# Optimization experiments

Measured on AMD Instinct MI355X. Metric: run time of the kernel, lower is better.

## Reference

```python
import jax, jax.numpy as jnp
import numpy as np

B_SZ = 16
L = 256
D_MODEL = 256
D_STATE = 16
D_CONV = 4
EXPAND = 2
D_INNER = EXPAND * D_MODEL  # 512
DT_RANK = (D_MODEL + 15) // 16  # 16
TARGET_LEN = 16


def setup_inputs() -> dict:
    key = jax.random.key(0)
    ks = jax.random.split(key, 10)
    s = 0.02
    x = jax.random.normal(ks[0], (B_SZ, D_MODEL, L), dtype=jnp.float32)
    W_in = jax.random.normal(ks[1], (2 * D_INNER, D_MODEL), dtype=jnp.float32) * s
    conv_w = jax.random.normal(ks[2], (D_INNER, D_CONV), dtype=jnp.float32) * s
    conv_b = jax.random.normal(ks[3], (D_INNER,), dtype=jnp.float32) * s
    W_x = jax.random.normal(ks[4], (DT_RANK + 2 * D_STATE, D_INNER), dtype=jnp.float32) * s
    W_dt = jax.random.normal(ks[5], (D_INNER, DT_RANK), dtype=jnp.float32) * s
    b_dt = jax.random.normal(ks[6], (D_INNER,), dtype=jnp.float32) * s
    # canonical Mamba A init: A_log = log(1..d_state) per channel
    A_log = jnp.log(jnp.tile(jnp.arange(1, D_STATE + 1, dtype=jnp.float32), (D_INNER, 1)))
    Dp = jnp.ones((D_INNER,), dtype=jnp.float32)
    W_out = jax.random.normal(ks[7], (D_MODEL, D_INNER), dtype=jnp.float32) * s
    return {"x": x, "W_in": W_in, "conv_w": conv_w, "conv_b": conv_b,
            "W_x": W_x, "W_dt": W_dt, "b_dt": b_dt, "A_log": A_log,
            "Dp": Dp, "W_out": W_out}


def _selective_scan(u, delta, A, Bm, Cm, Dp):
    # u, delta: [B,L,d_in]; Bm, Cm: [B,L,N]; A: [d_in,N]; Dp: [d_in]
    dA = jnp.exp(delta[..., None] * A)                                  # [B,L,d_in,N]
    dBu = delta[..., None] * Bm[:, :, None, :] * u[..., None]           # [B,L,d_in,N]

    def step(h, t):
        dA_t, dBu_t, C_t = t                                            # [B,d_in,N],[B,d_in,N],[B,N]
        h = dA_t * h + dBu_t
        y = jnp.einsum('bdn,bn->bd', h, C_t)
        return h, y

    h0 = jnp.zeros((u.shape[0], u.shape[2], A.shape[1]), u.dtype)
    _, ys = jax.lax.scan(step, h0,
                         (dA.transpose(1, 0, 2, 3), dBu.transpose(1, 0, 2, 3),
                          Cm.transpose(1, 0, 2)))
    return ys.transpose(1, 0, 2) + u * Dp                               # [B,L,d_in]


def _mamba(xt, W_in, conv_w, conv_b, W_x, W_dt, b_dt, A_log, Dp, W_out):
    # xt: [B,L,D_MODEL]
    xz = xt @ W_in.T                                                    # [B,L,2*d_in]
    xi, z = jnp.split(xz, 2, axis=-1)
    # causal depthwise conv1d over L
    xc = xi.transpose(0, 2, 1)                                          # [B,d_in,L]
    xc = jax.lax.conv_general_dilated(
        xc, conv_w[:, None, :], (1,), [(D_CONV - 1, 0)],
        dimension_numbers=('NCH', 'OIH', 'NCH'), feature_group_count=D_INNER)
    xi = jax.nn.silu((xc + conv_b[None, :, None]).transpose(0, 2, 1))   # [B,L,d_in]
    x_dbl = xi @ W_x.T                                                  # [B,L,dt_rank+2N]
    dt, Bm, Cm = jnp.split(x_dbl, [DT_RANK, DT_RANK + D_STATE], axis=-1)
    delta = jax.nn.softplus(dt @ W_dt.T + b_dt)                         # [B,L,d_in]
    A = -jnp.exp(A_log)                                                 # [d_in,N]
    y = _selective_scan(xi, delta, A, Bm, Cm, Dp)
    y = y * jax.nn.silu(z)
    return y @ W_out.T                                                  # [B,L,D_MODEL]


def reference(x, W_in, conv_w, conv_b, W_x, W_dt, b_dt, A_log, Dp, W_out):
    inp = x.transpose(0, 2, 1)                                          # [B,L,D]
    outs = []
    for _ in range(TARGET_LEN):
        o = _mamba(inp, W_in, conv_w, conv_b, W_x, W_dt, b_dt, A_log, Dp, W_out)[:, -1:, :]
        outs.append(o)
        inp = jnp.concatenate([inp[:, 1:, :], o], axis=1)
    return jnp.concatenate(outs, axis=1).transpose(0, 2, 1)             # [B,D,target_len]
```

## Files before the change

### kernel.cpp

```cpp
#include <hip/hip_runtime.h>
#include <cmath>

#define DEV __device__ __forceinline__

constexpr int B_SZ = 16;
constexpr int LSEQ = 256;
constexpr int DM   = 256;
constexpr int DI   = 512;
constexpr int TLEN = 16;

DEV float silu_f(float x)     { return x / (1.f + __expf(-x)); }
DEV float softplus_f(float x) { return log1pf(__expf(x)); }

__global__ __launch_bounds__(256) void k_fold(const float* __restrict__ W_in,
                                              const float* __restrict__ W_out,
                                              float* __restrict__ Wc) {
    __shared__ float As[32][68];
    __shared__ float Bs[32][68];
    const int j0 = blockIdx.y * 64;
    const int d0 = blockIdx.x * 64;
    const int tid = threadIdx.x;
    const int ty = tid >> 4, tx = tid & 15;
    float acc[4][4] = {};
    for (int kc = 0; kc < DM; kc += 32) {
        for (int it = 0; it < 8; ++it) {
            int idx = it * 256 + tid;
            int jj = idx >> 5, kk = idx & 31;
            As[kk][jj] = W_in[(size_t)(j0 + jj) * DM + kc + kk];
        }
        for (int it = 0; it < 8; ++it) {
            int idx = it * 256 + tid;
            int kk = idx >> 6, dd = idx & 63;
            Bs[kk][dd] = W_out[(size_t)(kc + kk) * DI + d0 + dd];
        }
        __syncthreads();
        for (int kk = 0; kk < 32; ++kk) {
            float4 a4 = *(const float4*)&As[kk][ty * 4];
            float4 b4 = *(const float4*)&Bs[kk][tx * 4];
            float av[4] = {a4.x, a4.y, a4.z, a4.w};
            float bv[4] = {b4.x, b4.y, b4.z, b4.w};
            for (int i = 0; i < 4; ++i)
                for (int j = 0; j < 4; ++j) acc[i][j] = fmaf(av[i], bv[j], acc[i][j]);
        }
        __syncthreads();
    }
    for (int i = 0; i < 4; ++i) {
        float4 v = make_float4(acc[i][0], acc[i][1], acc[i][2], acc[i][3]);
        *(float4*)&Wc[(size_t)(j0 + ty * 4 + i) * DI + d0 + tx * 4] = v;
    }
}

__global__ __launch_bounds__(256) void k_inproj(const float* __restrict__ x,
                                                const float* __restrict__ W_in,
                                                float* __restrict__ xi_pre) {
    __shared__ float As[32][68];
    __shared__ float Ws[32][68];
    const int by = blockIdx.y, bx = blockIdx.x;
    const int row0 = by * 64;
    const int b = row0 >> 8, l0 = row0 & 255;
    const int j0 = bx * 64;
    const int tid = threadIdx.x;
    const int ty = tid >> 4, tx = tid & 15;
    const float* xb = x + (size_t)b * DM * LSEQ;
    float acc[4][4] = {};
    for (int kc = 0; kc < DM; kc += 32) {
        for (int it = 0; it < 8; ++it) {
            int idx = it * 256 + tid;
            int kk = idx >> 6, li = idx & 63;
            As[kk][li] = xb[(kc + kk) * LSEQ + l0 + li];
        }
        for (int it = 0; it < 8; ++it) {
            int idx = it * 256 + tid;
            int jj = idx >> 5, kk = idx & 31;
            Ws[kk][jj] = W_in[(size_t)(j0 + jj) * DM + kc + kk];
        }
        __syncthreads();
        for (int kk = 0; kk < 32; ++kk) {
            float4 a4 = *(const float4*)&As[kk][ty * 4];
            float4 w4 = *(const float4*)&Ws[kk][tx * 4];
            float av[4] = {a4.x, a4.y, a4.z, a4.w};
            float wv[4] = {w4.x, w4.y, w4.z, w4.w};
            for (int i = 0; i < 4; ++i)
                for (int j = 0; j < 4; ++j) acc[i][j] = fmaf(av[i], wv[j], acc[i][j]);
        }
        __syncthreads();
    }
    for (int i = 0; i < 4; ++i) {
        float4 v = make_float4(acc[i][0], acc[i][1], acc[i][2], acc[i][3]);
        *(float4*)&xi_pre[(size_t)(row0 + ty * 4 + i) * DI + j0 + tx * 4] = v;
    }
}

__global__ __launch_bounds__(256) void k_z255(const float* __restrict__ x,
                                              const float* __restrict__ W_in,
                                              float* __restrict__ z255) {
    __shared__ __align__(16) float xcol[256];
    const int b = blockIdx.x >> 2, jq = blockIdx.x & 3;
    const int tid = threadIdx.x;
    xcol[tid] = x[(size_t)b * DM * LSEQ + tid * LSEQ + 255];
    __syncthreads();
    const int w = tid >> 6, lane = tid & 63;
    float4 xv = *(const float4*)&xcol[lane * 4];
    for (int rr = 0; rr < 32; ++rr) {
        const int j = jq * 128 + w * 32 + rr;
        float4 wv = *(const float4*)&W_in[(size_t)(DI + j) * DM + lane * 4];
        float s = wv.x * xv.x + wv.y * xv.y + wv.z * xv.z + wv.w * xv.w;
        for (int off = 32; off > 0; off >>= 1) s += __shfl_down(s, off);
        if (lane == 0) z255[b * DI + j] = s;
    }
}

__global__ __launch_bounds__(256) void k_dtbc(const float* __restrict__ xi_pre,
                                              const float* __restrict__ conv_w,
                                              const float* __restrict__ conv_b,
                                              const float* __restrict__ W_x,
                                              float* __restrict__ dtBC) {
    __shared__ float A2[35][65];
    __shared__ float As[32][65];
    __shared__ float Ws[48][65];
    __shared__ float cw_s[64][5];
    const int row0 = blockIdx.x * 32;
    const int b = row0 >> 8, l0 = row0 & 255;
    const int tid = threadIdx.x;
    const int r = tid >> 3, cg = tid & 7;
    float acc[6] = {};
    for (int kc = 0; kc < DI; kc += 64) {
        for (int it = 0; it < 9; ++it) {
            int idx = it * 256 + tid;
            if (idx < 2240) {
                int rr = idx >> 6, k = idx & 63;
                int l = l0 + rr - 3;
                A2[rr][k] = (l >= 0) ? xi_pre[(size_t)(b * 256 + l) * DI + kc + k] : 0.f;
            }
        }
        if (tid < 64) {
            for (int j = 0; j < 4; ++j) cw_s[tid][j] = conv_w[(kc + tid) * 4 + j];
            cw_s[tid][4] = conv_b[kc + tid];
        }
        for (int it = 0; it < 12; ++it) {
            int idx = it * 256 + tid;
            int c = idx >> 6, k = idx & 63;
            Ws[c][k] = W_x[(size_t)c * DI + kc + k];
        }
        __syncthreads();
        for (int it = 0; it < 8; ++it) {
            int idx = it * 256 + tid;
            int rr = idx >> 6, k = idx & 63;
            float s = cw_s[k][4];
            for (int j = 0; j < 4; ++j) s = fmaf(cw_s[k][j], A2[rr + j][k], s);
            As[rr][k] = silu_f(s);
        }
        __syncthreads();
        for (int kk = 0; kk < 64; ++kk) {
            float a = As[r][kk];
            for (int ci = 0; ci < 6; ++ci)
                acc[ci] = fmaf(a, Ws[cg * 6 + ci][kk], acc[ci]);
        }
        __syncthreads();
    }
    for (int ci = 0; ci < 6; ++ci)
        dtBC[(size_t)(row0 + r) * 48 + cg * 6 + ci] = acc[ci];
}

__global__ __launch_bounds__(512) void k_scan_chunk(const float* __restrict__ xi_pre,
                                                    const float* __restrict__ conv_w,
                                                    const float* __restrict__ conv_b,
                                                    const float* __restrict__ dtBC,
                                                    const float* __restrict__ W_dt,
                                                    const float* __restrict__ b_dt,
                                                    const float* __restrict__ A_log,
                                                    float* __restrict__ Qb,
                                                    float* __restrict__ Sb) {
    const int blk = blockIdx.x;
    const int b = blk >> 3, c = blk & 7;
    const int d = threadIdx.x;
    float Ar[16], Wd[16];
    for (int n = 0; n < 16; ++n) Ar[n] = -__expf(A_log[d * 16 + n]);
    for (int r = 0; r < 16; ++r) Wd[r] = W_dt[d * 16 + r];
    const float bd = b_dt[d];
    const float c0 = conv_w[d * 4 + 0], c1 = conv_w[d * 4 + 1];
    const float c2 = conv_w[d * 4 + 2], c3 = conv_w[d * 4 + 3];
    const float cbv = conv_b[d];
    const int lbase = c * 32;
    float p0, p1, p2;
    {
        int l;
        l = lbase - 3; p0 = (l >= 0) ? xi_pre[(size_t)(b * 256 + l) * DI + d] : 0.f;
        l = lbase - 2; p1 = (l >= 0) ? xi_pre[(size_t)(b * 256 + l) * DI + d] : 0.f;
        l = lbase - 1; p2 = (l >= 0) ? xi_pre[(size_t)(b * 256 + l) * DI + d] : 0.f;
    }
    float q[16] = {};
    float Ssum = 0.f;
    for (int l = lbase; l < lbase + 32; ++l) {
        const int rl = b * 256 + l;
        const float v = xi_pre[(size_t)rl * DI + d];
        const float u = silu_f(cbv + c0 * p0 + c1 * p1 + c2 * p2 + c3 * v);
        p0 = p1; p1 = p2; p2 = v;
        const float* dv = dtBC + (size_t)rl * 48;
        float s = bd;
        for (int r = 0; r < 16; ++r) s = fmaf(dv[r], Wd[r], s);
        const float del = softplus_f(s);
        const float du = del * u;
        Ssum += del;
        for (int n = 0; n < 16; ++n) {
            float dA = __expf(del * Ar[n]);
            q[n] = fmaf(dA, q[n], du * dv[16 + n]);
        }
    }
    float* qo = Qb + ((size_t)blk * DI + d) * 16;
    for (int n = 0; n < 16; ++n) qo[n] = q[n];
    Sb[blk * DI + d] = Ssum;
}

__global__ __launch_bounds__(512) void k_compose(const float* __restrict__ Qb,
                                                 const float* __restrict__ Sb,
                                                 const float* __restrict__ dtBC,
                                                 const float* __restrict__ xi_pre,
                                                 const float* __restrict__ conv_w,
                                                 const float* __restrict__ conv_b,
                                                 const float* __restrict__ z255,
                                                 const float* __restrict__ A_log,
                                                 const float* __restrict__ Dp,
                                                 float* __restrict__ h_state,
                                                 float* __restrict__ gbuf) {
    const int b = blockIdx.x;
    const int d = threadIdx.x;
    float Ar[16];
    for (int n = 0; n < 16; ++n) Ar[n] = -__expf(A_log[d * 16 + n]);
    float h[16] = {};
    for (int c = 0; c < 8; ++c) {
        const int blk = b * 8 + c;
        const float S = Sb[blk * DI + d];
        const float* qv = Qb + ((size_t)blk * DI + d) * 16;
        for (int n = 0; n < 16; ++n) {
            float P = __expf(S * Ar[n]);
            h[n] = fmaf(P, h[n], qv[n]);
        }
    }
    const float* Cv = dtBC + (size_t)(b * 256 + 255) * 48 + 32;
    float y = 0.f;
    for (int n = 0; n < 16; ++n) y = fmaf(h[n], Cv[n], y);
    float u;
    {
        float pv[4];
        for (int k = 0; k < 4; ++k) pv[k] = xi_pre[(size_t)(b * 256 + 252 + k) * DI + d];
        float s = conv_b[d];
        for (int k = 0; k < 4; ++k) s = fmaf(conv_w[d * 4 + k], pv[k], s);
        u = silu_f(s);
    }
    y = fmaf(u, Dp[d], y);
    gbuf[b * DI + d] = y * silu_f(z255[b * DI + d]);
    float* ho = h_state + ((size_t)(b * DI + d)) * 16;
    for (int n = 0; n < 16; ++n) ho[n] = h[n];
}

__global__ __launch_bounds__(512, 1) void k_gen(
    const float* __restrict__ Wc, const float* __restrict__ W_out,
    const float* __restrict__ W_x, const float* __restrict__ W_dt,
    const float* __restrict__ conv_w, const float* __restrict__ conv_b,
    const float* __restrict__ b_dt, const float* __restrict__ A_log,
    const float* __restrict__ Dp, const float* __restrict__ xi_pre,
    const float* __restrict__ h_state, const float* __restrict__ gbuf0,
    float* __restrict__ xbuf, unsigned* __restrict__ flags,
    float* __restrict__ out) {
    const int bid = blockIdx.x;
    const int b = bid & 15;
    const int p = bid >> 4;
    const int tid = threadIdx.x;

    __shared__ float wc_s[64][513];
    __shared__ float wx_s[48][33];
    __shared__ float gs_s[512];
    __shared__ float xin_s[512];
    __shared__ float zs_s[512];
    __shared__ float dpart[16][49];
    __shared__ float dtbc_s[48];
    __shared__ float red8[8][65];
    __shared__ float hist[3][32];
    __shared__ float post_s[112];

    for (int i = 0; i < 16; ++i) {
        int flat = i * 512 + tid;
        int rr = flat >> 7;
        int c4 = (flat & 127) * 4;
        int gr = (rr < 32) ? (p * 32 + rr) : (DI + p * 32 + (rr - 32));
        float4 v = *(const float4*)&Wc[(size_t)gr * DI + c4];
        wc_s[rr][c4 + 0] = v.x; wc_s[rr][c4 + 1] = v.y;
        wc_s[rr][c4 + 2] = v.z; wc_s[rr][c4 + 3] = v.w;
    }
    for (int i = 0; i < 3; ++i) {
        int flat = i * 512 + tid;
        int rr = flat >> 5, cc = flat & 31;
        wx_s[rr][cc] = W_x[(size_t)rr * DI + p * 32 + cc];
    }
    const int orow = p * 16 + (tid >> 5), osub = tid & 31;
    float wout[16];
    #pragma unroll
    for (int j = 0; j < 16; ++j) wout[j] = W_out[(size_t)orow * DI + osub + 32 * j];

    float wdt[16], Ar[16], h[16];
    {
        const float4* wp = (const float4*)&W_dt[tid * 16];
        const float4* ap = (const float4*)&A_log[tid * 16];
        const float4* hp = (const float4*)&h_state[((size_t)(b * DI + tid)) * 16];
        #pragma unroll
        for (int i = 0; i < 4; ++i) {
            float4 wv = wp[i], av = ap[i], hv = hp[i];
            wdt[4*i+0]=wv.x; wdt[4*i+1]=wv.y; wdt[4*i+2]=wv.z; wdt[4*i+3]=wv.w;
            Ar[4*i+0]=-__expf(av.x); Ar[4*i+1]=-__expf(av.y);
            Ar[4*i+2]=-__expf(av.z); Ar[4*i+3]=-__expf(av.w);
            h[4*i+0]=hv.x; h[4*i+1]=hv.y; h[4*i+2]=hv.z; h[4*i+3]=hv.w;
        }
    }
    const float bd = b_dt[tid];
    const float Dpv = Dp[tid];
    float cw0 = 0, cw1 = 0, cw2 = 0, cw3 = 0, cb = 0;
    if (tid < 32) {
        const int d = p * 32 + tid;
        cw0 = conv_w[d * 4 + 0]; cw1 = conv_w[d * 4 + 1];
        cw2 = conv_w[d * 4 + 2]; cw3 = conv_w[d * 4 + 3];
        cb  = conv_b[d];
        for (int k = 0; k < 3; ++k)
            hist[k][tid] = xi_pre[(size_t)(b * 256 + 253 + k) * DI + d];
    }
    gs_s[tid] = gbuf0[b * DI + tid];
    __syncthreads();

    for (int t = 0; t < TLEN; ++t) {
        if (t < TLEN - 1) {
            {
                const int r = tid & 63, sub = tid >> 6;
                const float* wrow = &wc_s[r][sub * 64];
                const float* gv = &gs_s[sub * 64];
                float s = 0.f;
                #pragma unroll
                for (int k = 0; k < 64; ++k) s = fmaf(wrow[k], gv[k], s);
                red8[sub][r] = s;
            }
            __syncthreads();
            if (tid < 64) {
                float v = 0.f;
                #pragma unroll
                for (int ss = 0; ss < 8; ++ss) v += red8[ss][tid];
                if (tid < 32) {
                    float xc = cb;
                    xc = fmaf(cw0, hist[t % 3][tid], xc);
                    xc = fmaf(cw1, hist[(t + 1) % 3][tid], xc);
                    xc = fmaf(cw2, hist[(t + 2) % 3][tid], xc);
                    xc = fmaf(cw3, v, xc);
                    hist[t % 3][tid] = v;
                    post_s[tid] = silu_f(xc);
                } else {
                    post_s[tid] = v;
                }
            }
            __syncthreads();
            if (tid < 384) {
                const int r = tid >> 3, sub = tid & 7;
                const float* wr = &wx_s[r][sub * 4];
                const float* xv = &post_s[sub * 4];
                float s = wr[0]*xv[0] + wr[1]*xv[1] + wr[2]*xv[2] + wr[3]*xv[3];
                s += __shfl_down(s, 4); s += __shfl_down(s, 2); s += __shfl_down(s, 1);
                if (sub == 0) post_s[64 + r] = s;
            }
            __syncthreads();
            if (tid < 112) {
                float* slot = xbuf + ((size_t)((b * 16 + p) * 2 + (t & 1))) * 128;
                __hip_atomic_store(&slot[tid], post_s[tid],
                                   __ATOMIC_RELAXED, __HIP_MEMORY_SCOPE_AGENT);
            }
            __syncthreads();
            if (tid == 256)
                __hip_atomic_store(&flags[(b * 16 + p) * 16], (unsigned)(t + 1),
                                   __ATOMIC_RELEASE, __HIP_MEMORY_SCOPE_AGENT);
        }
        {
            float s = 0.f;
            #pragma unroll
            for (int j = 0; j < 16; ++j) s = fmaf(wout[j], gs_s[osub + 32 * j], s);
            s += __shfl_down(s, 16); s += __shfl_down(s, 8);
            s += __shfl_down(s, 4);  s += __shfl_down(s, 2); s += __shfl_down(s, 1);
            if (osub == 0) out[(size_t)(b * 256 + orow) * TLEN + t] = s;
        }
        if (t == TLEN - 1) return;

        if (tid < 16) {
            while (__hip_atomic_load(&flags[(b * 16 + tid) * 16],
                                     __ATOMIC_ACQUIRE, __HIP_MEMORY_SCOPE_AGENT)
                   < (unsigned)(t + 1))
                __builtin_amdgcn_s_sleep(1);
        }
        __syncthreads();
        for (int i = 0; i < 4; ++i) {
            int idx = i * 512 + tid;
            int q = idx >> 7, pos = idx & 127;
            if (pos < 112) {
                float v = __hip_atomic_load(
                    xbuf + ((size_t)((b * 16 + q) * 2 + (t & 1))) * 128 + pos,
                    __ATOMIC_RELAXED, __HIP_MEMORY_SCOPE_AGENT);
                if (pos < 32)      xin_s[q * 32 + pos] = v;
                else if (pos < 64) zs_s[q * 32 + pos - 32] = v;
                else               dpart[q][pos - 64] = v;
            }
        }
        __syncthreads();
        if (tid < 48) {
            float s = 0.f;
            #pragma unroll
            for (int q = 0; q < 16; ++q) s += dpart[q][tid];
            dtbc_s[tid] = s;
        }
        __syncthreads();
        {
            float dt_l = bd;
            #pragma unroll
            for (int r = 0; r < 16; ++r) dt_l = fmaf(dtbc_s[r], wdt[r], dt_l);
            const float del = softplus_f(dt_l);
            const float u = xin_s[tid];
            const float du = del * u;
            float y = 0.f;
            #pragma unroll
            for (int n = 0; n < 16; ++n) {
                float dA = __expf(del * Ar[n]);
                h[n] = fmaf(dA, h[n], du * dtbc_s[16 + n]);
                y = fmaf(h[n], dtbc_s[32 + n], y);
            }
            y = fmaf(u, Dpv, y);
            gs_s[tid] = y * silu_f(zs_s[tid]);
        }
        __syncthreads();
    }
}

extern "C" void kernel_launch(void* const* d_in, const int* in_sizes, int n_in,
                              void* d_out, int out_size, void* d_ws, size_t ws_size,
                              hipStream_t stream) {
    const float* x      = (const float*)d_in[0];
    const float* W_in   = (const float*)d_in[1];
    const float* conv_w = (const float*)d_in[2];
    const float* conv_b = (const float*)d_in[3];
    const float* W_x    = (const float*)d_in[4];
    const float* W_dt   = (const float*)d_in[5];
    const float* b_dt   = (const float*)d_in[6];
    const float* A_log  = (const float*)d_in[7];
    const float* Dp     = (const float*)d_in[8];
    const float* W_out  = (const float*)d_in[9];
    float* out = (float*)d_out;

    float* base = (float*)d_ws;
    size_t off = 0;
    auto alloc = [&](size_t n) { float* pp = base + off; off += (n + 15) & ~(size_t)15; return pp; };
    unsigned* flags = (unsigned*)alloc(256 * 16);
    float* xbuf     = alloc((size_t)16 * 16 * 2 * 128);
    float* gbuf     = alloc(16 * 512);
    float* h_state  = alloc((size_t)16 * 512 * 16);
    float* z255     = alloc(16 * 512);
    float* dtBC     = alloc((size_t)4096 * 48);
    float* Sb       = alloc((size_t)128 * 512);
    float* Qb       = alloc((size_t)128 * 512 * 16);
    float* xi_pre   = alloc((size_t)4096 * 512);
    float* Wc       = alloc((size_t)1024 * 512);

    hipMemsetAsync(flags, 0, 256 * 16 * sizeof(unsigned), stream);
    hipLaunchKernelGGL(k_fold, dim3(8, 16), dim3(256), 0, stream, W_in, W_out, Wc);
    hipLaunchKernelGGL(k_inproj, dim3(8, 64), dim3(256), 0, stream, x, W_in, xi_pre);
    hipLaunchKernelGGL(k_z255, dim3(64), dim3(256), 0, stream, x, W_in, z255);
    hipLaunchKernelGGL(k_dtbc, dim3(128), dim3(256), 0, stream,
                       xi_pre, conv_w, conv_b, W_x, dtBC);
    hipLaunchKernelGGL(k_scan_chunk, dim3(128), dim3(512), 0, stream,
                       xi_pre, conv_w, conv_b, dtBC, W_dt, b_dt, A_log, Qb, Sb);
    hipLaunchKernelGGL(k_compose, dim3(16), dim3(512), 0, stream,
                       Qb, Sb, dtBC, xi_pre, conv_w, conv_b, z255, A_log, Dp,
                       h_state, gbuf);
    hipLaunchKernelGGL(k_gen, dim3(256), dim3(512), 0, stream,
                       Wc, W_out, W_x, W_dt, conv_w, conv_b, b_dt, A_log, Dp,
                       xi_pre, h_state, gbuf, xbuf, flags, out);
}
```

Measured before the change: 358.3 us.

## Fuse prefill kernels and restructure generation step to compute x_proj redundantly per block

Merges the weight-fold and in-projection GEMMs into one launch, folds the dtBC projection into the chunked scan kernel, and moves the z255 computation into the compose stage. This cuts the prefill from six launches to three. In the generation loop, each block now keeps its folded-weight slice in registers from a transposed layout and recomputes the full W_x projection locally, so blocks exchange only 64 floats instead of partial sums. This shrinks the inter-block exchange and removes one barrier phase, at the cost of redundant x_proj work per block and more register pressure.

```diff
diff --git a/kernel.cpp b/kernel.cpp
--- a/kernel.cpp
+++ b/kernel.cpp
@@ -12,219 +12,203 @@
 DEV float silu_f(float x)     { return x / (1.f + __expf(-x)); }
 DEV float softplus_f(float x) { return log1pf(__expf(x)); }
 
-__global__ __launch_bounds__(256) void k_fold(const float* __restrict__ W_in,
-                                              const float* __restrict__ W_out,
-                                              float* __restrict__ Wc) {
-    __shared__ float As[32][68];
-    __shared__ float Bs[32][68];
-    const int j0 = blockIdx.y * 64;
-    const int d0 = blockIdx.x * 64;
+__global__ __launch_bounds__(256) void k_prefill_a(const float* __restrict__ x,
+                                                   const float* __restrict__ W_in,
+                                                   const float* __restrict__ W_out,
+                                                   float* __restrict__ WcT,
+                                                   float* __restrict__ xi_pre) {
+    __shared__ float smem[2][32][68];
     const int tid = threadIdx.x;
     const int ty = tid >> 4, tx = tid & 15;
     float acc[4][4] = {};
-    for (int kc = 0; kc < DM; kc += 32) {
-        for (int it = 0; it < 8; ++it) {
-            int idx = it * 256 + tid;
-            int jj = idx >> 5, kk = idx & 31;
-            As[kk][jj] = W_in[(size_t)(j0 + jj) * DM + kc + kk];
-        }
-        for (int it = 0; it < 8; ++it) {
-            int idx = it * 256 + tid;
-            int kk = idx >> 6, dd = idx & 63;
-            Bs[kk][dd] = W_out[(size_t)(kc + kk) * DI + d0 + dd];
-        }
+    if (blockIdx.x < 128) {
+        const int j0 = (int)(blockIdx.x & 15) * 64;
+        const int d0 = (int)(blockIdx.x >> 4) * 64;
+        float (*As)[68] = smem[0];
+        float (*Bs)[68] = smem[1];
+        for (int kc = 0; kc < DM; kc += 32) {
+            for (int it = 0; it < 8; ++it) {
+                int idx = it * 256 + tid;
+                int jj = idx >> 5, kk = idx & 31;
+                As[kk][jj] = W_in[(size_t)(j0 + jj) * DM + kc + kk];
+            }
+            for (int it = 0; it < 8; ++it) {
+                int idx = it * 256 + tid;
+                int kk = idx >> 6, dd = idx & 63;
+                Bs[kk][dd] = W_out[(size_t)(kc + kk) * DI + d0 + dd];
+            }
+            __syncthreads();
+            for (int kk = 0; kk < 32; ++kk) {
+                float4 a4 = *(const float4*)&As[kk][ty * 4];
+                float4 b4 = *(const float4*)&Bs[kk][tx * 4];
+                float av[4] = {a4.x, a4.y, a4.z, a4.w};
+                float bv[4] = {b4.x, b4.y, b4.z, b4.w};
+                for (int i = 0; i < 4; ++i)
+                    for (int j = 0; j < 4; ++j) acc[i][j] = fmaf(av[i], bv[j], acc[i][j]);
+            }
+            __syncthreads();
+        }
+        float (*Cs)[65] = (float(*)[65])&smem[0][0][0];
+        for (int i = 0; i < 4; ++i)
+            for (int j = 0; j < 4; ++j)
+                Cs[ty * 4 + i][tx * 4 + j] = acc[i][j];
         __syncthreads();
-        for (int kk = 0; kk < 32; ++kk) {
-            float4 a4 = *(const float4*)&As[kk][ty * 4];
-            float4 b4 = *(const float4*)&Bs[kk][tx * 4];
-            float av[4] = {a4.x, a4.y, a4.z, a4.w};
-            float bv[4] = {b4.x, b4.y, b4.z, b4.w};
-            for (int i = 0; i < 4; ++i)
-                for (int j = 0; j < 4; ++j) acc[i][j] = fmaf(av[i], bv[j], acc[i][j]);
-        }
-        __syncthreads();
-    }
-    for (int i = 0; i < 4; ++i) {
-        float4 v = make_float4(acc[i][0], acc[i][1], acc[i][2], acc[i][3]);
-        *(float4*)&Wc[(size_t)(j0 + ty * 4 + i) * DI + d0 + tx * 4] = v;
+        const int dr = tid >> 2, jq = tid & 3;
+        for (int ii = 0; ii < 4; ++ii) {
+            int jl = jq * 16 + ii * 4;
+            int jg = j0 + jl;
+            int newc;
+            if (jg < DI) newc = (jg >> 5) * 64 + (jg & 31);
+            else { int jz = jg - DI; newc = (jz >> 5) * 64 + 32 + (jz & 31); }
+            float4 v = make_float4(Cs[jl][dr], Cs[jl + 1][dr], Cs[jl + 2][dr], Cs[jl + 3][dr]);
+            *(float4*)&WcT[(size_t)(d0 + dr) * 1024 + newc] = v;
+        }
+    } else {
+        const int bid2 = (int)blockIdx.x - 128;
+        const int bx = bid2 & 7, by = bid2 >> 3;
+        const int row0 = by * 64;
+        const int b = row0 >> 8, l0 = row0 & 255;
+        const int j0 = bx * 64;
+        float (*As)[68] = smem[0];
+        float (*Ws)[68] = smem[1];
+        const float* xb = x + (size_t)b * DM * LSEQ;
+        for (int kc = 0; kc < DM; kc += 32) {
+            for (int it = 0; it < 8; ++it) {
+                int idx = it * 256 + tid;
+                int kk = idx >> 6, li = idx & 63;
+                As[kk][li] = xb[(kc + kk) * LSEQ + l0 + li];
+            }
+            for (int it = 0; it < 8; ++it) {
+                int idx = it * 256 + tid;
+                int jj = idx >> 5, kk = idx & 31;
+                Ws[kk][jj] = W_in[(size_t)(j0 + jj) * DM + kc + kk];
+            }
+            __syncthreads();
+            for (int kk = 0; kk < 32; ++kk) {
+                float4 a4 = *(const float4*)&As[kk][ty * 4];
+                float4 w4 = *(const float4*)&Ws[kk][tx * 4];
+                float av[4] = {a4.x, a4.y, a4.z, a4.w};
+                float wv[4] = {w4.x, w4.y, w4.z, w4.w};
+                for (int i = 0; i < 4; ++i)
+                    for (int j = 0; j < 4; ++j) acc[i][j] = fmaf(av[i], wv[j], acc[i][j]);
+            }
+            __syncthreads();
+        }
+        for (int i = 0; i < 4; ++i) {
+            float4 v = make_float4(acc[i][0], acc[i][1], acc[i][2], acc[i][3]);
+            *(float4*)&xi_pre[(size_t)(row0 + ty * 4 + i) * DI + j0 + tx * 4] = v;
+        }
     }
 }
 
-__global__ __launch_bounds__(256) void k_inproj(const float* __restrict__ x,
-                                                const float* __restrict__ W_in,
-                                                float* __restrict__ xi_pre) {
-    __shared__ float As[32][68];
-    __shared__ float Ws[32][68];
-    const int by = blockIdx.y, bx = blockIdx.x;
-    const int row0 = by * 64;
-    const int b = row0 >> 8, l0 = row0 & 255;
-    const int j0 = bx * 64;
-    const int tid = threadIdx.x;
-    const int ty = tid >> 4, tx = tid & 15;
-    const float* xb = x + (size_t)b * DM * LSEQ;
-    float acc[4][4] = {};
-    for (int kc = 0; kc < DM; kc += 32) {
-        for (int it = 0; it < 8; ++it) {
-            int idx = it * 256 + tid;
-            int kk = idx >> 6, li = idx & 63;
-            As[kk][li] = xb[(kc + kk) * LSEQ + l0 + li];
-        }
-        for (int it = 0; it < 8; ++it) {
-            int idx = it * 256 + tid;
-            int jj = idx >> 5, kk = idx & 31;
-            Ws[kk][jj] = W_in[(size_t)(j0 + jj) * DM + kc + kk];
-        }
-        __syncthreads();
-        for (int kk = 0; kk < 32; ++kk) {
-            float4 a4 = *(const float4*)&As[kk][ty * 4];
-            float4 w4 = *(const float4*)&Ws[kk][tx * 4];
-            float av[4] = {a4.x, a4.y, a4.z, a4.w};
-            float wv[4] = {w4.x, w4.y, w4.z, w4.w};
-            for (int i = 0; i < 4; ++i)
-                for (int j = 0; j < 4; ++j) acc[i][j] = fmaf(av[i], wv[j], acc[i][j]);
-        }
-        __syncthreads();
-    }
-    for (int i = 0; i < 4; ++i) {
-        float4 v = make_float4(acc[i][0], acc[i][1], acc[i][2], acc[i][3]);
-        *(float4*)&xi_pre[(size_t)(row0 + ty * 4 + i) * DI + j0 + tx * 4] = v;
-    }
-}
-
-__global__ __launch_bounds__(256) void k_z255(const float* __restrict__ x,
-                                              const float* __restrict__ W_in,
-                                              float* __restrict__ z255) {
-    __shared__ __align__(16) float xcol[256];
-    const int b = blockIdx.x >> 2, jq = blockIdx.x & 3;
-    const int tid = threadIdx.x;
-    xcol[tid] = x[(size_t)b * DM * LSEQ + tid * LSEQ + 255];
-    __syncthreads();
-    const int w = tid >> 6, lane = tid & 63;
-    float4 xv = *(const float4*)&xcol[lane * 4];
-    for (int rr = 0; rr < 32; ++rr) {
-        const int j = jq * 128 + w * 32 + rr;
-        float4 wv = *(const float4*)&W_in[(size_t)(DI + j) * DM + lane * 4];
-        float s = wv.x * xv.x + wv.y * xv.y + wv.z * xv.z + wv.w * xv.w;
-        for (int off = 32; off > 0; off >>= 1) s += __shfl_down(s, off);
-        if (lane == 0) z255[b * DI + j] = s;
-    }
-}
-
-__global__ __launch_bounds__(256) void k_dtbc(const float* __restrict__ xi_pre,
-                                              const float* __restrict__ conv_w,
-                                              const float* __restrict__ conv_b,
-                                              const float* __restrict__ W_x,
-                                              float* __restrict__ dtBC) {
-    __shared__ float A2[35][65];
-    __shared__ float As[32][65];
-    __shared__ float Ws[48][65];
-    __shared__ float cw_s[64][5];
-    const int row0 = blockIdx.x * 32;
-    const int b = row0 >> 8, l0 = row0 & 255;
-    const int tid = threadIdx.x;
-    const int r = tid >> 3, cg = tid & 7;
-    float acc[6] = {};
-    for (int kc = 0; kc < DI; kc += 64) {
-        for (int it = 0; it < 9; ++it) {
-            int idx = it * 256 + tid;
-            if (idx < 2240) {
-                int rr = idx >> 6, k = idx & 63;
-                int l = l0 + rr - 3;
-                A2[rr][k] = (l >= 0) ? xi_pre[(size_t)(b * 256 + l) * DI + kc + k] : 0.f;
-            }
-        }
-        if (tid < 64) {
-            for (int j = 0; j < 4; ++j) cw_s[tid][j] = conv_w[(kc + tid) * 4 + j];
-            cw_s[tid][4] = conv_b[kc + tid];
-        }
-        for (int it = 0; it < 12; ++it) {
-            int idx = it * 256 + tid;
-            int c = idx >> 6, k = idx & 63;
-            Ws[c][k] = W_x[(size_t)c * DI + kc + k];
-        }
-        __syncthreads();
-        for (int it = 0; it < 8; ++it) {
-            int idx = it * 256 + tid;
-            int rr = idx >> 6, k = idx & 63;
-            float s = cw_s[k][4];
-            for (int j = 0; j < 4; ++j) s = fmaf(cw_s[k][j], A2[rr + j][k], s);
-            As[rr][k] = silu_f(s);
-        }
-        __syncthreads();
-        for (int kk = 0; kk < 64; ++kk) {
-            float a = As[r][kk];
-            for (int ci = 0; ci < 6; ++ci)
-                acc[ci] = fmaf(a, Ws[cg * 6 + ci][kk], acc[ci]);
-        }
-        __syncthreads();
-    }
-    for (int ci = 0; ci < 6; ++ci)
-        dtBC[(size_t)(row0 + r) * 48 + cg * 6 + ci] = acc[ci];
-}
-
-__global__ __launch_bounds__(512) void k_scan_chunk(const float* __restrict__ xi_pre,
-                                                    const float* __restrict__ conv_w,
-                                                    const float* __restrict__ conv_b,
-                                                    const float* __restrict__ dtBC,
-                                                    const float* __restrict__ W_dt,
-                                                    const float* __restrict__ b_dt,
-                                                    const float* __restrict__ A_log,
-                                                    float* __restrict__ Qb,
-                                                    float* __restrict__ Sb) {
+__global__ __launch_bounds__(512) void k_prefill_b(const float* __restrict__ xi_pre,
+                                                   const float* __restrict__ conv_w,
+                                                   const float* __restrict__ conv_b,
+                                                   const float* __restrict__ W_x,
+                                                   const float* __restrict__ W_dt,
+                                                   const float* __restrict__ b_dt,
+                                                   const float* __restrict__ A_log,
+                                                   float* __restrict__ Qb,
+                                                   float* __restrict__ Sb,
+                                                   float* __restrict__ dtBC255) {
+    __shared__ float As[32][516];
+    __shared__ float Ws[48][129];
+    __shared__ float dt_s[32][49];
     const int blk = blockIdx.x;
     const int b = blk >> 3, c = blk & 7;
     const int d = threadIdx.x;
-    float Ar[16], Wd[16];
-    for (int n = 0; n < 16; ++n) Ar[n] = -__expf(A_log[d * 16 + n]);
-    for (int r = 0; r < 16; ++r) Wd[r] = W_dt[d * 16 + r];
-    const float bd = b_dt[d];
-    const float c0 = conv_w[d * 4 + 0], c1 = conv_w[d * 4 + 1];
-    const float c2 = conv_w[d * 4 + 2], c3 = conv_w[d * 4 + 3];
-    const float cbv = conv_b[d];
-    const int lbase = c * 32;
-    float p0, p1, p2;
-    {
+    const int l0 = c * 32;
+    {
+        const float c0 = conv_w[d * 4 + 0], c1 = conv_w[d * 4 + 1];
+        const float c2 = conv_w[d * 4 + 2], c3 = conv_w[d * 4 + 3];
+        const float cbv = conv_b[d];
+        float p0, p1, p2;
         int l;
-        l = lbase - 3; p0 = (l >= 0) ? xi_pre[(size_t)(b * 256 + l) * DI + d] : 0.f;
-        l = lbase - 2; p1 = (l >= 0) ? xi_pre[(size_t)(b * 256 + l) * DI + d] : 0.f;
-        l = lbase - 1; p2 = (l >= 0) ? xi_pre[(size_t)(b * 256 + l) * DI + d] : 0.f;
-    }
-    float q[16] = {};
-    float Ssum = 0.f;
-    for (int l = lbase; l < lbase + 32; ++l) {
-        const int rl = b * 256 + l;
-        const float v = xi_pre[(size_t)rl * DI + d];
-        const float u = silu_f(cbv + c0 * p0 + c1 * p1 + c2 * p2 + c3 * v);
-        p0 = p1; p1 = p2; p2 = v;
-        const float* dv = dtBC + (size_t)rl * 48;
-        float s = bd;
-        for (int r = 0; r < 16; ++r) s = fmaf(dv[r], Wd[r], s);
-        const float del = softplus_f(s);
-        const float du = del * u;
-        Ssum += del;
-        for (int n = 0; n < 16; ++n) {
-            float dA = __expf(del * Ar[n]);
-            q[n] = fmaf(dA, q[n], du * dv[16 + n]);
-        }
-    }
-    float* qo = Qb + ((size_t)blk * DI + d) * 16;
-    for (int n = 0; n < 16; ++n) qo[n] = q[n];
-    Sb[blk * DI + d] = Ssum;
+        l = l0 - 3; p0 = (l >= 0) ? xi_pre[(size_t)(b * 256 + l) * DI + d] : 0.f;
+        l = l0 - 2; p1 = (l >= 0) ? xi_pre[(size_t)(b * 256 + l) * DI + d] : 0.f;
+        l = l0 - 1; p2 = (l >= 0) ? xi_pre[(size_t)(b * 256 + l) * DI + d] : 0.f;
+        for (int ll = 0; ll < 32; ++ll) {
+            float v = xi_pre[(size_t)(b * 256 + l0 + ll) * DI + d];
+            As[ll][d] = silu_f(cbv + c0 * p0 + c1 * p1 + c2 * p2 + c3 * v);
+            p0 = p1; p1 = p2; p2 = v;
+        }
+    }
+    __syncthreads();
+    {
+        const int lr = d >> 4, rg = d & 15;
+        float acc[3] = {};
+        for (int kc = 0; kc < 4; ++kc) {
+            for (int it = 0; it < 12; ++it) {
+                int idx = it * 512 + d;
+                int rr = idx >> 7, k = idx & 127;
+                Ws[rr][k] = W_x[(size_t)rr * DI + kc * 128 + k];
+            }
+            __syncthreads();
+            for (int k = 0; k < 128; ++k) {
+                float a = As[lr][kc * 128 + k];
+                acc[0] = fmaf(a, Ws[rg * 3 + 0][k], acc[0]);
+                acc[1] = fmaf(a, Ws[rg * 3 + 1][k], acc[1]);
+                acc[2] = fmaf(a, Ws[rg * 3 + 2][k], acc[2]);
+            }
+            __syncthreads();
+        }
+        dt_s[lr][rg * 3 + 0] = acc[0];
+        dt_s[lr][rg * 3 + 1] = acc[1];
+        dt_s[lr][rg * 3 + 2] = acc[2];
+    }
+    __syncthreads();
+    {
+        float Ar[16], Wd[16];
+        for (int n = 0; n < 16; ++n) Ar[n] = -__expf(A_log[d * 16 + n]);
+        for (int r = 0; r < 16; ++r) Wd[r] = W_dt[d * 16 + r];
+        const float bd = b_dt[d];
+        float q[16] = {};
+        float Ssum = 0.f;
+        for (int l = 0; l < 32; ++l) {
+            float s = bd;
+            for (int r = 0; r < 16; ++r) s = fmaf(dt_s[l][r], Wd[r], s);
+            const float del = softplus_f(s);
+            const float u = As[l][d];
+            const float du = del * u;
+            Ssum += del;
+            for (int n = 0; n < 16; ++n) {
+                float dA = __expf(del * Ar[n]);
+                q[n] = fmaf(dA, q[n], du * dt_s[l][16 + n]);
+            }
+        }
+        float* qo = Qb + ((size_t)blk * DI + d) * 16;
+        for (int n = 0; n < 16; ++n) qo[n] = q[n];
+        Sb[blk * DI + d] = Ssum;
+    }
+    if (c == 7 && d < 48) dtBC255[b * 48 + d] = dt_s[31][d];
 }
 
-__global__ __launch_bounds__(512) void k_compose(const float* __restrict__ Qb,
-                                                 const float* __restrict__ Sb,
-                                                 const float* __restrict__ dtBC,
-                                                 const float* __restrict__ xi_pre,
-                                                 const float* __restrict__ conv_w,
-                                                 const float* __restrict__ conv_b,
-                                                 const float* __restrict__ z255,
-                                                 const float* __restrict__ A_log,
-                                                 const float* __restrict__ Dp,
-                                                 float* __restrict__ h_state,
-                                                 float* __restrict__ gbuf) {
+__global__ __launch_bounds__(512) void k_prefill_c(const float* __restrict__ x,
+                                                   const float* __restrict__ W_in,
+                                                   const float* __restrict__ Qb,
+                                                   const float* __restrict__ Sb,
+                                                   const float* __restrict__ dtBC255,
+                                                   const float* __restrict__ xi_pre,
+                                                   const float* __restrict__ conv_w,
+                                                   const float* __restrict__ conv_b,
+                                                   const float* __restrict__ A_log,
+                                                   const float* __restrict__ Dp,
+                                                   float* __restrict__ h_state,
+                                                   float* __restrict__ gbuf) {
+    __shared__ __align__(16) float xcol[256];
     const int b = blockIdx.x;
     const int d = threadIdx.x;
+    if (d < 256) xcol[d] = x[(size_t)b * DM * LSEQ + d * LSEQ + 255];
+    __syncthreads();
+    float z = 0.f;
+    {
+        const float4* wr = (const float4*)&W_in[(size_t)(DI + d) * DM];
+        const float4* xc4 = (const float4*)xcol;
+        for (int k = 0; k < 64; ++k) {
+            float4 w = wr[k], xx = xc4[k];
+            z += w.x * xx.x + w.y * xx.y + w.z * xx.z + w.w * xx.w;
+        }
+    }
     float Ar[16];
     for (int n = 0; n < 16; ++n) Ar[n] = -__expf(A_log[d * 16 + n]);
     float h[16] = {};
@@ -237,25 +221,23 @@
             h[n] = fmaf(P, h[n], qv[n]);
         }
     }
-    const float* Cv = dtBC + (size_t)(b * 256 + 255) * 48 + 32;
     float y = 0.f;
-    for (int n = 0; n < 16; ++n) y = fmaf(h[n], Cv[n], y);
+    for (int n = 0; n < 16; ++n) y = fmaf(h[n], dtBC255[b * 48 + 32 + n], y);
     float u;
     {
-        float pv[4];
-        for (int k = 0; k < 4; ++k) pv[k] = xi_pre[(size_t)(b * 256 + 252 + k) * DI + d];
         float s = conv_b[d];
-        for (int k = 0; k < 4; ++k) s = fmaf(conv_w[d * 4 + k], pv[k], s);
+        for (int k = 0; k < 4; ++k)
+            s = fmaf(conv_w[d * 4 + k], xi_pre[(size_t)(b * 256 + 252 + k) * DI + d], s);
         u = silu_f(s);
     }
     y = fmaf(u, Dp[d], y);
-    gbuf[b * DI + d] = y * silu_f(z255[b * DI + d]);
+    gbuf[b * DI + d] = y * silu_f(z);
     float* ho = h_state + ((size_t)(b * DI + d)) * 16;
     for (int n = 0; n < 16; ++n) ho[n] = h[n];
 }
 
-__global__ __launch_bounds__(512, 1) void k_gen(
-    const float* __restrict__ Wc, const float* __restrict__ W_out,
+__global__ __launch_bounds__(512) void k_gen(
+    const float* __restrict__ WcT, const float* __restrict__ W_out,
     const float* __restrict__ W_x, const float* __restrict__ W_dt,
     const float* __restrict__ conv_w, const float* __restrict__ conv_b,
     const float* __restrict__ b_dt, const float* __restrict__ A_log,
@@ -268,30 +250,24 @@
     const int p = bid >> 4;
     const int tid = threadIdx.x;
 
-    __shared__ float wc_s[64][513];
-    __shared__ float wx_s[48][33];
+    __shared__ float wx_s[48][516];
     __shared__ float gs_s[512];
     __shared__ float xin_s[512];
     __shared__ float zs_s[512];
-    __shared__ float dpart[16][49];
+    __shared__ float red8[8][65];
     __shared__ float dtbc_s[48];
-    __shared__ float red8[8][65];
     __shared__ float hist[3][32];
-    __shared__ float post_s[112];
-
-    for (int i = 0; i < 16; ++i) {
-        int flat = i * 512 + tid;
-        int rr = flat >> 7;
-        int c4 = (flat & 127) * 4;
-        int gr = (rr < 32) ? (p * 32 + rr) : (DI + p * 32 + (rr - 32));
-        float4 v = *(const float4*)&Wc[(size_t)gr * DI + c4];
-        wc_s[rr][c4 + 0] = v.x; wc_s[rr][c4 + 1] = v.y;
-        wc_s[rr][c4 + 2] = v.z; wc_s[rr][c4 + 3] = v.w;
-    }
-    for (int i = 0; i < 3; ++i) {
-        int flat = i * 512 + tid;
-        int rr = flat >> 5, cc = flat & 31;
-        wx_s[rr][cc] = W_x[(size_t)rr * DI + p * 32 + cc];
+
+    const int r = tid & 63, w = tid >> 6;
+    float wc[64];
+    {
+        const float* src = WcT + (size_t)(w * 64) * 1024 + p * 64 + r;
+        #pragma unroll
+        for (int kk = 0; kk < 64; ++kk) wc[kk] = src[(size_t)kk * 1024];
+    }
+    for (int it = 0; it < 48; ++it) {
+        int flat = it * 512 + tid;
+        wx_s[flat >> 9][flat & 511] = W_x[flat];
     }
     const int orow = p * 16 + (tid >> 5), osub = tid & 31;
     float wout[16];
@@ -329,19 +305,24 @@
     for (int t = 0; t < TLEN; ++t) {
         if (t < TLEN - 1) {
             {
-                const int r = tid & 63, sub = tid >> 6;
-                const float* wrow = &wc_s[r][sub * 64];
-                const float* gv = &gs_s[sub * 64];
+                const float4* g4 = (const float4*)&gs_s[w * 64];
                 float s = 0.f;
                 #pragma unroll
-                for (int k = 0; k < 64; ++k) s = fmaf(wrow[k], gv[k], s);
-                red8[sub][r] = s;
+                for (int kk = 0; kk < 16; ++kk) {
+                    float4 g = g4[kk];
+                    s = fmaf(wc[4*kk+0], g.x, s);
+                    s = fmaf(wc[4*kk+1], g.y, s);
+                    s = fmaf(wc[4*kk+2], g.z, s);
+                    s = fmaf(wc[4*kk+3], g.w, s);
+                }
+                red8[w][r] = s;
             }
             __syncthreads();
             if (tid < 64) {
                 float v = 0.f;
                 #pragma unroll
                 for (int ss = 0; ss < 8; ++ss) v += red8[ss][tid];
+                float outv;
                 if (tid < 32) {
                     float xc = cb;
                     xc = fmaf(cw0, hist[t % 3][tid], xc);
@@ -349,29 +330,16 @@
                     xc = fmaf(cw2, hist[(t + 2) % 3][tid], xc);
                     xc = fmaf(cw3, v, xc);
                     hist[t % 3][tid] = v;
-                    post_s[tid] = silu_f(xc);
+                    outv = silu_f(xc);
                 } else {
-                    post_s[tid] = v;
+                    outv = v;
                 }
-            }
-            __syncthreads();
-            if (tid < 384) {
-                const int r = tid >> 3, sub = tid & 7;
-                const float* wr = &wx_s[r][sub * 4];
-                const float* xv = &post_s[sub * 4];
-                float s = wr[0]*xv[0] + wr[1]*xv[1] + wr[2]*xv[2] + wr[3]*xv[3];
-                s += __shfl_down(s, 4); s += __shfl_down(s, 2); s += __shfl_down(s, 1);
-                if (sub == 0) post_s[64 + r] = s;
-            }
-            __syncthreads();
-            if (tid < 112) {
-                float* slot = xbuf + ((size_t)((b * 16 + p) * 2 + (t & 1))) * 128;
-                __hip_atomic_store(&slot[tid], post_s[tid],
-                                   __ATOMIC_RELAXED, __HIP_MEMORY_SCOPE_AGENT);
-            }
-            __syncthreads();
-            if (tid == 256)
-                __hip_atomic_store(&flags[(b * 16 + p) * 16], (unsigned)(t + 1),
+                __hip_atomic_store(&xbuf[((size_t)((b * 16 + p) * 2 + (t & 1))) * 64 + tid],
+                                   outv, __ATOMIC_RELAXED, __HIP_MEMORY_SCOPE_AGENT);
+            }
+            __syncthreads();
+            if (tid == 0)
+                __hip_atomic_store(&flags[b * 16 + p], (unsigned)(t + 1),
                                    __ATOMIC_RELEASE, __HIP_MEMORY_SCOPE_AGENT);
         }
         {
@@ -385,36 +353,38 @@
         if (t == TLEN - 1) return;
 
         if (tid < 16) {
-            while (__hip_atomic_load(&flags[(b * 16 + tid) * 16],
+            while (__hip_atomic_load(&flags[b * 16 + tid],
                                      __ATOMIC_ACQUIRE, __HIP_MEMORY_SCOPE_AGENT)
                    < (unsigned)(t + 1))
                 __builtin_amdgcn_s_sleep(1);
         }
         __syncthreads();
-        for (int i = 0; i < 4; ++i) {
+        #pragma unroll
+        for (int i = 0; i < 2; ++i) {
             int idx = i * 512 + tid;
-            int q = idx >> 7, pos = idx & 127;
-            if (pos < 112) {
-                float v = __hip_atomic_load(
-                    xbuf + ((size_t)((b * 16 + q) * 2 + (t & 1))) * 128 + pos,
-                    __ATOMIC_RELAXED, __HIP_MEMORY_SCOPE_AGENT);
-                if (pos < 32)      xin_s[q * 32 + pos] = v;
-                else if (pos < 64) zs_s[q * 32 + pos - 32] = v;
-                else               dpart[q][pos - 64] = v;
-            }
+            int q = idx >> 6, pos = idx & 63;
+            float v = __hip_atomic_load(
+                xbuf + ((size_t)((b * 16 + q) * 2 + (t & 1))) * 64 + pos,
+                __ATOMIC_RELAXED, __HIP_MEMORY_SCOPE_AGENT);
+            if (pos < 32) xin_s[q * 32 + pos] = v;
+            else          zs_s[q * 32 + pos - 32] = v;
         }
         __syncthreads();
-        if (tid < 48) {
+        if (tid < 384) {
+            const int rr = tid >> 3, sub = tid & 7;
+            const float* wr = &wx_s[rr][sub * 64];
+            const float* xv = &xin_s[sub * 64];
             float s = 0.f;
             #pragma unroll
-            for (int q = 0; q < 16; ++q) s += dpart[q][tid];
-            dtbc_s[tid] = s;
+            for (int k = 0; k < 64; ++k) s = fmaf(wr[k], xv[k], s);
+            s += __shfl_down(s, 4); s += __shfl_down(s, 2); s += __shfl_down(s, 1);
+            if (sub == 0) dtbc_s[rr] = s;
         }
         __syncthreads();
         {
             float dt_l = bd;
             #pragma unroll
-            for (int r = 0; r < 16; ++r) dt_l = fmaf(dtbc_s[r], wdt[r], dt_l);
+            for (int rr = 0; rr < 16; ++rr) dt_l = fmaf(dtbc_s[rr], wdt[rr], dt_l);
             const float del = softplus_f(dt_l);
             const float u = xin_s[tid];
             const float du = del * u;
@@ -450,29 +420,25 @@
     float* base = (float*)d_ws;
     size_t off = 0;
     auto alloc = [&](size_t n) { float* pp = base + off; off += (n + 15) & ~(size_t)15; return pp; };
-    unsigned* flags = (unsigned*)alloc(256 * 16);
-    float* xbuf     = alloc((size_t)16 * 16 * 2 * 128);
+    unsigned* flags = (unsigned*)alloc(256);
+    float* xbuf     = alloc((size_t)16 * 16 * 2 * 64);
     float* gbuf     = alloc(16 * 512);
     float* h_state  = alloc((size_t)16 * 512 * 16);
-    float* z255     = alloc(16 * 512);
-    float* dtBC     = alloc((size_t)4096 * 48);
+    float* dtBC255  = alloc(16 * 48);
     float* Sb       = alloc((size_t)128 * 512);
     float* Qb       = alloc((size_t)128 * 512 * 16);
     float* xi_pre   = alloc((size_t)4096 * 512);
-    float* Wc       = alloc((size_t)1024 * 512);
-
-    hipMemsetAsync(flags, 0, 256 * 16 * sizeof(unsigned), stream);
-    hipLaunchKernelGGL(k_fold, dim3(8, 16), dim3(256), 0, stream, W_in, W_out, Wc);
-    hipLaunchKernelGGL(k_inproj, dim3(8, 64), dim3(256), 0, stream, x, W_in, xi_pre);
-    hipLaunchKernelGGL(k_z255, dim3(64), dim3(256), 0, stream, x, W_in, z255);
-    hipLaunchKernelGGL(k_dtbc, dim3(128), dim3(256), 0, stream,
-                       xi_pre, conv_w, conv_b, W_x, dtBC);
-    hipLaunchKernelGGL(k_scan_chunk, dim3(128), dim3(512), 0, stream,
-                       xi_pre, conv_w, conv_b, dtBC, W_dt, b_dt, A_log, Qb, Sb);
-    hipLaunchKernelGGL(k_compose, dim3(16), dim3(512), 0, stream,
-                       Qb, Sb, dtBC, xi_pre, conv_w, conv_b, z255, A_log, Dp,
+    float* WcT      = alloc((size_t)512 * 1024);
+
+    hipMemsetAsync(flags, 0, 256 * sizeof(unsigned), stream);
+    hipLaunchKernelGGL(k_prefill_a, dim3(640), dim3(256), 0, stream,
+                       x, W_in, W_out, WcT, xi_pre);
+    hipLaunchKernelGGL(k_prefill_b, dim3(128), dim3(512), 0, stream,
+                       xi_pre, conv_w, conv_b, W_x, W_dt, b_dt, A_log, Qb, Sb, dtBC255);
+    hipLaunchKernelGGL(k_prefill_c, dim3(16), dim3(512), 0, stream,
+                       x, W_in, Qb, Sb, dtBC255, xi_pre, conv_w, conv_b, A_log, Dp,
                        h_state, gbuf);
     hipLaunchKernelGGL(k_gen, dim3(256), dim3(512), 0, stream,
-                       Wc, W_out, W_x, W_dt, conv_w, conv_b, b_dt, A_log, Dp,
+                       WcT, W_out, W_x, W_dt, conv_w, conv_b, b_dt, A_log, Dp,
                        xi_pre, h_state, gbuf, xbuf, flags, out);
 }
```

Measured after the change: 357.3 us. Within noise of the previous version (-0.3%).
